# Performance work log

Hardware: AMD Instinct MI355X
Metric: run time of the kernel (lower is better)

Reference implementation:

```python
import jax, jax.numpy as jnp
import numpy as np


def _elem_mlp(x, w1, b1, w2, b2):
    # elementwise 1 -> N -> 1 ReLU MLP (distilled exp / inv approximators)
    h = jax.nn.relu(x[..., None] * w1[:, 0] + b1)  # [..., N]
    return jnp.einsum('...n,n->...', h, w2[0]) + b2[0]


def setup_inputs() -> dict:
    key = jax.random.key(0)
    ks = jax.random.split(key, 13)
    T, S, B, D = 8, 512, 8, 512
    NE, NI = 32, 64
    f = jnp.float32
    inp = {
        'sx': jax.random.normal(ks[0], (T, S, B, D), f) * 0.1,
        'q_proj_weight': jax.random.normal(ks[1], (D, D), f) / np.sqrt(D),
        'k_proj_weight': jax.random.normal(ks[2], (D, D), f) / np.sqrt(D),
        'q_proj_bias': jax.random.normal(ks[3], (D,), f) * 0.02,
        'k_proj_bias': jax.random.normal(ks[4], (D,), f) * 0.02,
        'exp_w1': jax.random.normal(ks[5], (NE, 1), f),
        'exp_b1': jax.random.normal(ks[6], (NE,), f) * 0.1,
        'exp_w2': jax.random.normal(ks[7], (1, NE), f) / np.sqrt(NE),
        'exp_b2': jax.random.normal(ks[8], (1,), f) * 0.01,
        'inv_w1': jax.random.normal(ks[9], (NI, 1), f),
        'inv_b1': jax.random.normal(ks[10], (NI,), f) * 0.1,
        'inv_w2': jax.random.normal(ks[11], (1, NI), f) / np.sqrt(NI),
        'inv_b2': jax.random.normal(ks[12], (1,), f) * 0.01,
        'num_heads': 8,
    }
    return inp


def reference(sx, q_proj_weight, k_proj_weight, q_proj_bias, k_proj_bias,
              exp_w1, exp_b1, exp_w2, exp_b2,
              inv_w1, inv_b1, inv_w2, inv_b2, num_heads):
    T, S, B, D = sx.shape
    H = num_heads
    hd = D // H
    scale = 1.0 / np.sqrt(hd)

    def proj(x_t, W, b):
        # [S, B, D] -> [B*H, S, hd]
        y = x_t @ W.T + b
        return y.reshape(S, B * H, hd).transpose(1, 0, 2)

    def step(carry, x_t):
        sum_q, sum_k, sum_p = carry
        sq = proj(x_t, q_proj_weight, q_proj_bias)
        sk = proj(x_t, k_proj_weight, k_proj_bias)
        sum_q = sum_q + sq
        # sp_t = sum_q @ sk^T + sq @ sum_k^T (sum_k updated AFTER, per snn_qk_product)
        sp = (jnp.einsum('bsh,bth->bst', sum_q, sk)
              + jnp.einsum('bsh,bth->bst', sq, sum_k)) * scale
        sum_k = sum_k + sk
        return (sum_q, sum_k, sum_p + sp), None

    z_qk = jnp.zeros((B * H, S, hd), sx.dtype)
    z_p = jnp.zeros((B * H, S, S), sx.dtype)
    (sum_q, sum_k, sum_p), _ = jax.lax.scan(step, (z_qk, z_qk, z_p), sx)

    p = sum_p / T  # time-averaged accumulated QK product

    # fit_softmax: distilled-MLP softmax approximation
    tmax = p[:, :, 0:1]
    tp = jnp.minimum(p - (tmax - 1.0), 3.0)
    x_up = jnp.where(tp > -20.0,
                     _elem_mlp(tp, exp_w1, exp_b1, exp_w2, exp_b2), 0.0)
    partition = x_up.sum(-1, keepdims=True)
    p_inv = _elem_mlp(partition, inv_w1, inv_b1, inv_w2, inv_b2)
    out = x_up * p_inv
    partition_p2 = out.sum(-1, keepdims=True)
    p_inv2 = _elem_mlp(partition_p2, inv_w1, inv_b1, inv_w2, inv_b2)
    out2 = jnp.where(partition_p2 > 1.5, out * p_inv2, out)
    return out2
```

## Files before the change

kernel.cpp:

```cpp
#include <hip/hip_runtime.h>


#define T_  8
#define NE_ 32
#define NI_ 64

#define LUT_N   2048
#define LUT_LO  -20.0f
#define LUT_HI  3.0f
#define LUT_INVW (LUT_N / (LUT_HI - LUT_LO))
#define LUT_W    ((LUT_HI - LUT_LO) / LUT_N)

typedef __attribute__((ext_vector_type(8))) short bf16x8;
typedef __attribute__((ext_vector_type(4))) float f32x4;
typedef __attribute__((ext_vector_type(4))) unsigned int u32x4;

#define XS_OFF 0u
#define WQ_OFF 2097152u
#define WK_OFF 2359296u
#define QB_OFF 2621440u
#define KB_OFF 4718592u
#define LUT_OFF 6815744u

__device__ inline unsigned short f2bf(float f) {
  union { float f; unsigned u; } v; v.f = f;
  unsigned r = v.u + 0x7FFFu + ((v.u >> 16) & 1u);
  return (unsigned short)(r >> 16);
}

__device__ inline void gload16(const void* g, void* l) {
  __builtin_amdgcn_global_load_lds(
      (const __attribute__((address_space(1))) void*)g,
      (__attribute__((address_space(3))) void*)l, 16, 0, 0);
}

__device__ inline bf16x8 lds_read_swz(const unsigned short* base, int row, int byteoff) {
  int addr = row * 128 + (byteoff ^ ((row & 7) << 4));
  return *(const bf16x8*)((const char*)base + addr);
}

__device__ inline float invmlp4(float x, const float* __restrict__ w1,
                                const float* __restrict__ b1,
                                const float* __restrict__ w2, float b2) {
  float a0 = b2, a1 = 0.f, a2 = 0.f, a3 = 0.f;
#pragma unroll
  for (int n = 0; n < NI_; n += 4) {
    a0 += w2[n + 0] * fmaxf(x * w1[n + 0] + b1[n + 0], 0.0f);
    a1 += w2[n + 1] * fmaxf(x * w1[n + 1] + b1[n + 1], 0.0f);
    a2 += w2[n + 2] * fmaxf(x * w1[n + 2] + b1[n + 2], 0.0f);
    a3 += w2[n + 3] * fmaxf(x * w1[n + 3] + b1[n + 3], 0.0f);
  }
  return (a0 + a1) + (a2 + a3);
}

__device__ inline float expmlp_exact(float t, const float* __restrict__ w1,
                                     const float* __restrict__ b1,
                                     const float* __restrict__ w2, float b2) {
  float a = b2;
#pragma unroll
  for (int n = 0; n < NE_; n++) a += w2[n] * fmaxf(t * w1[n] + b1[n], 0.0f);
  return a;
}

__global__ __launch_bounds__(256) void k_pre(
    const float* __restrict__ sx, const float* __restrict__ wq,
    const float* __restrict__ wk, const float* __restrict__ ew1,
    const float* __restrict__ eb1, const float* __restrict__ ew2,
    const float* __restrict__ eb2p,
    unsigned short* __restrict__ xs, unsigned short* __restrict__ wqb,
    unsigned short* __restrict__ wkb, float2* __restrict__ lut) {
  int bx = blockIdx.x, tid = threadIdx.x;
  if (bx < 2048) {
    size_t i = ((size_t)bx * 256 + tid) * 4;
    f32x4 a = __builtin_nontemporal_load((const f32x4*)(sx + i));
#pragma unroll
    for (int t = 1; t < T_; t++) {
      f32x4 v = __builtin_nontemporal_load((const f32x4*)(sx + (size_t)t * 2097152 + i));
      a += v;
    }
    ushort4 o; o.x = f2bf(a[0]); o.y = f2bf(a[1]); o.z = f2bf(a[2]); o.w = f2bf(a[3]);
    *(ushort4*)(xs + i) = o;
  } else if (bx < 2560) {
    const float* src = (bx < 2304) ? wq : wk;
    unsigned short* dst = (bx < 2304) ? wqb : wkb;
    int base = (bx < 2304) ? 2048 : 2304;
    size_t i = ((size_t)(bx - base) * 256 + tid) * 4;
    float4 a = *(const float4*)(src + i);
    ushort4 o; o.x = f2bf(a.x); o.y = f2bf(a.y); o.z = f2bf(a.z); o.w = f2bf(a.w);
    *(ushort4*)(dst + i) = o;
  } else {
    int i = (bx - 2560) * 256 + tid;
    if (i < LUT_N) {
      float b2 = eb2p[0];
      float tl = fmaf((float)i, LUT_W, LUT_LO);
      float th = fmaf((float)(i + 1), LUT_W, LUT_LO);
      float el = expmlp_exact(tl, ew1, eb1, ew2, b2);
      float eh = expmlp_exact(th, ew1, eb1, ew2, b2);
      float alpha = (eh - el) * LUT_INVW;
      float beta = fmaf(-alpha, tl, el);
      lut[i] = make_float2(alpha, beta);
    }
  }
}

__global__ __launch_bounds__(256, 2) void k_proj(
    const unsigned short* __restrict__ xs, const unsigned short* __restrict__ wb,
    const float* __restrict__ bq, const float* __restrict__ bk,
    unsigned short* __restrict__ outb) {
  __shared__ unsigned short Sh[2][128 * 64];
  int tid = threadIdx.x;
  int lane = tid & 63, w = tid >> 6;
  int r0 = blockIdx.x * 128;
  int c0 = blockIdx.y * 128;
  int z = blockIdx.z;
  const unsigned short* W = wb + (size_t)z * 262144;
  const float* bias = z ? bk : bq;
  unsigned short* dst = outb + (size_t)z * 2097152;
  float sc = z ? 1.0f : (1.0f / 64.0f);

  int rgrp = lane >> 4, cl = lane & 15;
  int r0w = (w >> 1) * 64, c0w = (w & 1) * 64;

  f32x4 acc[4][4];
  f32x4 zero = {0.f, 0.f, 0.f, 0.f};
#pragma unroll
  for (int m = 0; m < 4; m++)
#pragma unroll
    for (int n = 0; n < 4; n++) acc[m][n] = zero;

  int rl = lane >> 3, slot = lane & 7;

  for (int kt = 0; kt < 8; kt++) {
    int k0 = kt * 64;
#pragma unroll
    for (int i = 0; i < 4; i++) {
      int chunk = w * 4 + i;
      int r = chunk * 8 + rl;
      int sw = (slot ^ (r & 7)) * 8;
      gload16(xs + (size_t)(r0 + r) * 512 + k0 + sw, (char*)Sh[0] + chunk * 1024);
      gload16(W + (size_t)(c0 + r) * 512 + k0 + sw, (char*)Sh[1] + chunk * 1024);
    }
    __syncthreads();
#pragma unroll
    for (int kb = 0; kb < 2; kb++) {
      bf16x8 af[4], bfr[4];
#pragma unroll
      for (int m = 0; m < 4; m++) af[m] = lds_read_swz(Sh[0], r0w + 16 * m + cl, kb * 64 + rgrp * 16);
#pragma unroll
      for (int n = 0; n < 4; n++) bfr[n] = lds_read_swz(Sh[1], c0w + 16 * n + cl, kb * 64 + rgrp * 16);
#pragma unroll
      for (int m = 0; m < 4; m++)
#pragma unroll
        for (int n = 0; n < 4; n++)
          acc[m][n] = __builtin_amdgcn_mfma_f32_16x16x32_bf16(af[m], bfr[n], acc[m][n], 0, 0, 0);
    }
    __syncthreads();
  }

  unsigned short* Os = &Sh[0][0];
#pragma unroll
  for (int n = 0; n < 4; n++) {
    int cgl = c0w + 16 * n + cl;
    float bv = 8.0f * bias[c0 + cgl];
    int h = cgl >> 6, dh = cgl & 63;
    int hh = dh >> 5, rg2 = (dh >> 3) & 3, jj = dh & 7;
#pragma unroll
    for (int m = 0; m < 4; m++) {
#pragma unroll
      for (int j = 0; j < 4; j++) {
        int rgl = r0w + 16 * m + rgrp * 4 + j;
        int sl = rgl >> 3, b = rgl & 7;
        Os[(((b * 2 + h) * 2 + hh) * 512) + (rg2 * 16 + sl) * 8 + jj] =
            f2bf((acc[m][n][j] + bv) * sc);
      }
    }
  }
  __syncthreads();

  int cb = r0 >> 7;
  int h0 = c0 >> 6;
#pragma unroll
  for (int i = 0; i < 8; i++) {
    int unit = i * 256 + tid;
    int b = unit >> 8, h = (unit >> 7) & 1, hh = (unit >> 6) & 1, inner = unit & 63;
    int bh = b * 8 + h0 + h;
    size_t du = ((size_t)((bh * 32 + cb) * 2 + hh)) * 512 + inner * 8;
    *(u32x4*)(dst + du) = *(const u32x4*)(Os + unit * 8);
  }
}

__global__ __launch_bounds__(256, 4) void k_attn(
    const unsigned short* __restrict__ qb, const unsigned short* __restrict__ kb,
    const float2* __restrict__ lutg,
    const float* __restrict__ iw1, const float* __restrict__ ib1,
    const float* __restrict__ iw2, const float* __restrict__ ib2p,
    float* __restrict__ out) {
  __shared__ float2 Lut[LUT_N];
  __shared__ float s_part[4][16];
  __shared__ float s_fac[16];

  int tid = threadIdx.x;
  int lane = tid & 63, w = tid >> 6;
  int i = blockIdx.x;
  int xcd = i & 7, j2 = i >> 3;
  int bh = xcd * 8 + (j2 >> 5);
  int rb = j2 & 31;
  int rgrp = lane >> 4, cl = lane & 15;

#pragma unroll
  for (int c = 0; c < 4; c++) {
    int chunk = w * 4 + c;
    gload16((const char*)lutg + chunk * 1024 + lane * 16, (char*)Lut + chunk * 1024);
  }

  const char* Qb = (const char*)qb + (size_t)((bh * 32 + rb) * 2) * 1024;
  bf16x8 aF0 = *(const bf16x8*)(Qb + lane * 16);
  bf16x8 aF1 = *(const bf16x8*)(Qb + 1024 + lane * 16);

  const char* Kbase = (const char*)kb + (size_t)(bh * 32) * 2048;
  f32x4 zero = {0.f, 0.f, 0.f, 0.f};

  float tm1[4];
  {
    bf16x8 b0 = *(const bf16x8*)(Kbase + lane * 16);
    bf16x8 b1 = *(const bf16x8*)(Kbase + 1024 + lane * 16);
    f32x4 p0 = __builtin_amdgcn_mfma_f32_16x16x32_bf16(aF0, b0, zero, 0, 0, 0);
    p0 = __builtin_amdgcn_mfma_f32_16x16x32_bf16(aF1, b1, p0, 0, 0, 0);
    int src = lane & 48;
#pragma unroll
    for (int j = 0; j < 4; j++) tm1[j] = __shfl(p0[j], src) - 1.0f;
  }

  f32x4 acc[8];
#pragma unroll
  for (int f = 0; f < 8; f++) {
    const char* Kb = Kbase + (size_t)(w * 8 + f) * 2048;
    bf16x8 b0 = *(const bf16x8*)(Kb + lane * 16);
    bf16x8 b1 = *(const bf16x8*)(Kb + 1024 + lane * 16);
    acc[f] = __builtin_amdgcn_mfma_f32_16x16x32_bf16(aF0, b0, zero, 0, 0, 0);
    acc[f] = __builtin_amdgcn_mfma_f32_16x16x32_bf16(aF1, b1, acc[f], 0, 0, 0);
  }

  __syncthreads();

  const float C0 = -LUT_LO * LUT_INVW;
  float rowsum[4] = {0.f, 0.f, 0.f, 0.f};
#pragma unroll
  for (int f = 0; f < 8; f++) {
#pragma unroll
    for (int j = 0; j < 4; j++) {
      float tp = fminf(acc[f][j] - tm1[j], 3.0f);
      float u = fmaf(tp, LUT_INVW, C0);
      u = fminf(fmaxf(u, 0.0f), (float)(LUT_N - 1));
      float2 ab = Lut[(int)u];
      float xu = fmaf(ab.x, tp, ab.y);
      xu = (tp > -20.0f) ? xu : 0.0f;
      acc[f][j] = xu;
      rowsum[j] += xu;
    }
  }

#pragma unroll
  for (int j = 0; j < 4; j++) {
    float s = rowsum[j];
    s += __shfl_xor(s, 1);
    s += __shfl_xor(s, 2);
    s += __shfl_xor(s, 4);
    s += __shfl_xor(s, 8);
    if (cl == 0) s_part[w][rgrp * 4 + j] = s;
  }
  __syncthreads();

  if (tid < 16) {
    float part = s_part[0][tid] + s_part[1][tid] + s_part[2][tid] + s_part[3][tid];
    float b2 = ib2p[0];
    float fac = invmlp4(part, iw1, ib1, iw2, b2);
    float pp2 = part * fac;
    if (pp2 > 1.5f) fac *= invmlp4(pp2, iw1, ib1, iw2, b2);
    s_fac[tid] = fac;
  }
  __syncthreads();

  float* outb = out + ((size_t)bh * 512 + rb * 16) * 512;
#pragma unroll
  for (int j = 0; j < 4; j++) {
    int row = rgrp * 4 + j;
    float fac = s_fac[row];
#pragma unroll
    for (int f = 0; f < 8; f++)
      __builtin_nontemporal_store(acc[f][j] * fac,
          &outb[(size_t)row * 512 + w * 128 + 16 * f + cl]);
  }
}

extern "C" void kernel_launch(void* const* d_in, const int* in_sizes, int n_in,
                              void* d_out, int out_size, void* d_ws, size_t ws_size,
                              hipStream_t stream) {
  (void)in_sizes; (void)n_in; (void)out_size; (void)ws_size;
  const float* sx  = (const float*)d_in[0];
  const float* wq  = (const float*)d_in[1];
  const float* wk  = (const float*)d_in[2];
  const float* bq  = (const float*)d_in[3];
  const float* bk  = (const float*)d_in[4];
  const float* ew1 = (const float*)d_in[5];
  const float* eb1 = (const float*)d_in[6];
  const float* ew2 = (const float*)d_in[7];
  const float* eb2 = (const float*)d_in[8];
  const float* iw1 = (const float*)d_in[9];
  const float* ib1 = (const float*)d_in[10];
  const float* iw2 = (const float*)d_in[11];
  const float* ib2 = (const float*)d_in[12];
  unsigned short* wsu = (unsigned short*)d_ws;
  float2* lut = (float2*)(wsu + LUT_OFF);
  float* out = (float*)d_out;

  k_pre<<<2568, 256, 0, stream>>>(sx, wq, wk, ew1, eb1, ew2, eb2,
                                  wsu + XS_OFF, wsu + WQ_OFF, wsu + WK_OFF, lut);
  k_proj<<<dim3(32, 4, 2), 256, 0, stream>>>(wsu + XS_OFF, wsu + WQ_OFF, bq, bk, wsu + QB_OFF);
  k_attn<<<2048, 256, 0, stream>>>(wsu + QB_OFF, wsu + KB_OFF, lut,
                                   iw1, ib1, iw2, ib2, out);
}
```

Measured before the change: 58.99 us.

## Halve projection row tile for more blocks; rebase LUT to index-space interpolation

The projection GEMM now uses 64-row tiles instead of 128, doubling the grid to 512 blocks so more CUs are busy, with the scatter-to-head layout indices rewritten to match. The softmax LUT stores slope and intercept in index units, so the attention kernel folds the max-subtraction and scaling into one FMA per element and interpolates directly on the index. This saves several ALU ops per element. The smaller tile lowers reuse of the weight tile, and the clamp at 3.0 now happens in index space.

After: 56.62 us. -4.0%, faster.

```diff
diff --git a/kernel.cpp b/kernel.cpp
--- a/kernel.cpp
+++ b/kernel.cpp
@@ -96,9 +96,9 @@
       float th = fmaf((float)(i + 1), LUT_W, LUT_LO);
       float el = expmlp_exact(tl, ew1, eb1, ew2, b2);
       float eh = expmlp_exact(th, ew1, eb1, ew2, b2);
-      float alpha = (eh - el) * LUT_INVW;
-      float beta = fmaf(-alpha, tl, el);
-      lut[i] = make_float2(alpha, beta);
+      float ap = eh - el;
+      float bp = fmaf(-ap, (float)i, el);
+      lut[i] = make_float2(ap, bp);
     }
   }
 }
@@ -107,10 +107,11 @@
     const unsigned short* __restrict__ xs, const unsigned short* __restrict__ wb,
     const float* __restrict__ bq, const float* __restrict__ bk,
     unsigned short* __restrict__ outb) {
-  __shared__ unsigned short Sh[2][128 * 64];
+  __shared__ unsigned short As[64 * 64];
+  __shared__ unsigned short Bs[128 * 64];
   int tid = threadIdx.x;
   int lane = tid & 63, w = tid >> 6;
-  int r0 = blockIdx.x * 128;
+  int r0 = blockIdx.x * 64;
   int c0 = blockIdx.y * 128;
   int z = blockIdx.z;
   const unsigned short* W = wb + (size_t)z * 262144;
@@ -119,12 +120,12 @@
   float sc = z ? 1.0f : (1.0f / 64.0f);
 
   int rgrp = lane >> 4, cl = lane & 15;
-  int r0w = (w >> 1) * 64, c0w = (w & 1) * 64;
-
-  f32x4 acc[4][4];
+  int r0w = (w >> 1) * 32, c0w = (w & 1) * 64;
+
+  f32x4 acc[2][4];
   f32x4 zero = {0.f, 0.f, 0.f, 0.f};
 #pragma unroll
-  for (int m = 0; m < 4; m++)
+  for (int m = 0; m < 2; m++)
 #pragma unroll
     for (int n = 0; n < 4; n++) acc[m][n] = zero;
 
@@ -132,24 +133,30 @@
 
   for (int kt = 0; kt < 8; kt++) {
     int k0 = kt * 64;
+#pragma unroll
+    for (int i = 0; i < 2; i++) {
+      int chunk = w * 2 + i;
+      int r = chunk * 8 + rl;
+      int sw = (slot ^ (r & 7)) * 8;
+      gload16(xs + (size_t)(r0 + r) * 512 + k0 + sw, (char*)As + chunk * 1024);
+    }
 #pragma unroll
     for (int i = 0; i < 4; i++) {
       int chunk = w * 4 + i;
       int r = chunk * 8 + rl;
       int sw = (slot ^ (r & 7)) * 8;
-      gload16(xs + (size_t)(r0 + r) * 512 + k0 + sw, (char*)Sh[0] + chunk * 1024);
-      gload16(W + (size_t)(c0 + r) * 512 + k0 + sw, (char*)Sh[1] + chunk * 1024);
+      gload16(W + (size_t)(c0 + r) * 512 + k0 + sw, (char*)Bs + chunk * 1024);
     }
     __syncthreads();
 #pragma unroll
     for (int kb = 0; kb < 2; kb++) {
-      bf16x8 af[4], bfr[4];
-#pragma unroll
-      for (int m = 0; m < 4; m++) af[m] = lds_read_swz(Sh[0], r0w + 16 * m + cl, kb * 64 + rgrp * 16);
-#pragma unroll
-      for (int n = 0; n < 4; n++) bfr[n] = lds_read_swz(Sh[1], c0w + 16 * n + cl, kb * 64 + rgrp * 16);
-#pragma unroll
-      for (int m = 0; m < 4; m++)
+      bf16x8 af[2], bfr[4];
+#pragma unroll
+      for (int m = 0; m < 2; m++) af[m] = lds_read_swz(As, r0w + 16 * m + cl, kb * 64 + rgrp * 16);
+#pragma unroll
+      for (int n = 0; n < 4; n++) bfr[n] = lds_read_swz(Bs, c0w + 16 * n + cl, kb * 64 + rgrp * 16);
+#pragma unroll
+      for (int m = 0; m < 2; m++)
 #pragma unroll
         for (int n = 0; n < 4; n++)
           acc[m][n] = __builtin_amdgcn_mfma_f32_16x16x32_bf16(af[m], bfr[n], acc[m][n], 0, 0, 0);
@@ -157,34 +164,36 @@
     __syncthreads();
   }
 
-  unsigned short* Os = &Sh[0][0];
+  unsigned short* Os = Bs;
 #pragma unroll
   for (int n = 0; n < 4; n++) {
     int cgl = c0w + 16 * n + cl;
     float bv = 8.0f * bias[c0 + cgl];
-    int h = cgl >> 6, dh = cgl & 63;
+    int hl = cgl >> 6, dh = cgl & 63;
     int hh = dh >> 5, rg2 = (dh >> 3) & 3, jj = dh & 7;
 #pragma unroll
-    for (int m = 0; m < 4; m++) {
+    for (int m = 0; m < 2; m++) {
 #pragma unroll
       for (int j = 0; j < 4; j++) {
         int rgl = r0w + 16 * m + rgrp * 4 + j;
-        int sl = rgl >> 3, b = rgl & 7;
-        Os[(((b * 2 + h) * 2 + hh) * 512) + (rg2 * 16 + sl) * 8 + jj] =
+        int b = rgl & 7, clsl = rgl >> 3;
+        Os[((((b * 2 + hl) * 2 + hh) * 4 + rg2) * 8 + clsl) * 8 + jj] =
             f2bf((acc[m][n][j] + bv) * sc);
       }
     }
   }
   __syncthreads();
 
-  int cb = r0 >> 7;
+  int cb = blockIdx.x >> 1;
+  int clsbase = (blockIdx.x & 1) * 8;
   int h0 = c0 >> 6;
 #pragma unroll
-  for (int i = 0; i < 8; i++) {
-    int unit = i * 256 + tid;
-    int b = unit >> 8, h = (unit >> 7) & 1, hh = (unit >> 6) & 1, inner = unit & 63;
-    int bh = b * 8 + h0 + h;
-    size_t du = ((size_t)((bh * 32 + cb) * 2 + hh)) * 512 + inner * 8;
+  for (int i2 = 0; i2 < 4; i2++) {
+    int unit = i2 * 256 + tid;
+    int clsl = unit & 7, rg2 = (unit >> 3) & 3, hh = (unit >> 5) & 1;
+    int hl = (unit >> 6) & 1, b = unit >> 7;
+    int bh = b * 8 + h0 + hl;
+    size_t du = ((size_t)((bh * 32 + cb) * 2 + hh)) * 512 + (rg2 * 16 + clsbase + clsl) * 8;
     *(u32x4*)(dst + du) = *(const u32x4*)(Os + unit * 8);
   }
 }
@@ -244,17 +253,22 @@
   __syncthreads();
 
   const float C0 = -LUT_LO * LUT_INVW;
+  float cj[4];
+#pragma unroll
+  for (int j = 0; j < 4; j++) cj[j] = fmaf(-tm1[j], LUT_INVW, C0);
+
   float rowsum[4] = {0.f, 0.f, 0.f, 0.f};
 #pragma unroll
   for (int f = 0; f < 8; f++) {
 #pragma unroll
     for (int j = 0; j < 4; j++) {
-      float tp = fminf(acc[f][j] - tm1[j], 3.0f);
-      float u = fmaf(tp, LUT_INVW, C0);
-      u = fminf(fmaxf(u, 0.0f), (float)(LUT_N - 1));
-      float2 ab = Lut[(int)u];
-      float xu = fmaf(ab.x, tp, ab.y);
-      xu = (tp > -20.0f) ? xu : 0.0f;
+      float u0 = fmaf(acc[f][j], LUT_INVW, cj[j]);
+      float u = fminf(fmaxf(u0, 0.0f), (float)LUT_N);
+      int bi = (int)u;
+      bi = min(bi, LUT_N - 1);
+      float2 ab = Lut[bi];
+      float xu = fmaf(ab.x, u, ab.y);
+      xu = (u0 > 0.0f) ? xu : 0.0f;
       acc[f][j] = xu;
       rowsum[j] += xu;
     }
@@ -316,7 +330,7 @@
 
   k_pre<<<2568, 256, 0, stream>>>(sx, wq, wk, ew1, eb1, ew2, eb2,
                                   wsu + XS_OFF, wsu + WQ_OFF, wsu + WK_OFF, lut);
-  k_proj<<<dim3(32, 4, 2), 256, 0, stream>>>(wsu + XS_OFF, wsu + WQ_OFF, bq, bk, wsu + QB_OFF);
+  k_proj<<<dim3(64, 4, 2), 256, 0, stream>>>(wsu + XS_OFF, wsu + WQ_OFF, bq, bk, wsu + QB_OFF);
   k_attn<<<2048, 256, 0, stream>>>(wsu + QB_OFF, wsu + KB_OFF, lut,
                                    iw1, ib1, iw2, ib2, out);
 }
```
